# Kernel tuning notes

Hardware: AMD Instinct MI355X
Metric: run time of the kernel (lower is better)

Reference implementation:

```python
import jax, jax.numpy as jnp
import numpy as np
import math

N_HEADS = 16

def _ln(x, g, b, eps=1e-5):
    m = jnp.mean(x, axis=-1, keepdims=True)
    v = jnp.var(x, axis=-1, keepdims=True)
    return (x - m) * jax.lax.rsqrt(v + eps) * g + b

def _block(x, ln1_g, ln1_b, ln2_g, ln2_b, wqkv, wo, w1, w2):
    b, k, d = x.shape
    dh = d // N_HEADS
    h = _ln(x, ln1_g, ln1_b)
    qkv = (h @ wqkv).reshape(b, k, 3, N_HEADS, dh)
    q, kk, v = qkv[:, :, 0], qkv[:, :, 1], qkv[:, :, 2]
    scores = jnp.einsum('bqhd,bkhd->bhqk', q, kk) / math.sqrt(dh)
    attn = jax.nn.softmax(scores, axis=-1)
    o = jnp.einsum('bhqk,bkhd->bqhd', attn, v).reshape(b, k, d) @ wo
    x = x + o
    h2 = _ln(x, ln2_g, ln2_b)
    return x + jax.nn.gelu(h2 @ w1) @ w2

def setup_inputs() -> dict:
    key = jax.random.key(0)
    ks = jax.random.split(key, 6)
    b, s, d, dff = 4, 4096, 1024, 4096
    sc = 0.02
    return {
        'x': jax.random.normal(ks[0], (b, s, d), jnp.float32),
        'router_w': jax.random.normal(ks[1], (d,), jnp.float32) * sc,
        'ln1_g': jnp.ones((d,), jnp.float32),
        'ln1_b': jnp.zeros((d,), jnp.float32),
        'ln2_g': jnp.ones((d,), jnp.float32),
        'ln2_b': jnp.zeros((d,), jnp.float32),
        'wqkv': jax.random.normal(ks[2], (d, 3 * d), jnp.float32) * sc,
        'wo': jax.random.normal(ks[3], (d, d), jnp.float32) * sc,
        'w1': jax.random.normal(ks[4], (d, dff), jnp.float32) * sc,
        'w2': jax.random.normal(ks[5], (dff, d), jnp.float32) * sc,
    }

def reference(x, router_w, ln1_g, ln1_b, ln2_g, ln2_b, wqkv, wo, w1, w2):
    b, s, d = x.shape
    K = s // 2  # top_k = int(s * capacity_factor), capacity_factor = 0.5
    logits = x @ router_w                      # [b, s]
    w, idx = jax.lax.top_k(logits, K)          # [b, K]
    order = jnp.argsort(idx, axis=1)           # sort selected tokens by position
    sel = jnp.take_along_axis(idx, order, axis=1)          # [b, K] sorted indices
    fx = jnp.take_along_axis(x, sel[..., None], axis=1)    # gather routed tokens [b, K, d]
    xo = _block(fx, ln1_g, ln1_b, ln2_g, ln2_b, wqkv, wo, w1, w2)
    rw = jnp.take_along_axis(jax.nn.softmax(w, axis=1), order, axis=1)[..., None]  # [b, K, 1]
    batch_idx = jnp.arange(b)[:, None]
    out = x.at[batch_idx, sel].add(rw * xo)    # softmax-weighted scatter-add
    return out
```

## Files before the change

kernel.cpp:

```cpp
#include <hip/hip_runtime.h>
#include <hip/hip_bf16.h>
#include <stdint.h>

typedef __hip_bfloat16 bf16;
typedef __attribute__((ext_vector_type(8))) short short8;
typedef __attribute__((ext_vector_type(4))) float f32x4;

#define B_   4
#define S_   4096
#define D_   1024
#define KSEL 2048
#define DFF  4096
#define NH   16
#define DH   64

static __device__ __forceinline__ void load_lds16(const void* g, void* l) {
  __builtin_amdgcn_global_load_lds((const __attribute__((address_space(1))) void*)g,
                                   (__attribute__((address_space(3))) void*)l,
                                   16, 0, 0);
}

static __device__ __forceinline__ short8 scale8(short8 v, float s) {
  short8 r;
#pragma unroll
  for (int i = 0; i < 8; ++i) {
    unsigned u = ((unsigned)(unsigned short)v[i]) << 16;
    float f = __uint_as_float(u) * s;
    bf16 o = __float2bfloat16(f);
    short t;
    __builtin_memcpy(&t, &o, 2);
    r[i] = t;
  }
  return r;
}

__global__ __launch_bounds__(256)
void copy_router(const float* __restrict__ x, const float* __restrict__ rwts,
                 float* __restrict__ out, float* __restrict__ logits)
{
  int s = blockIdx.x, b = blockIdx.y;
  int tid = threadIdx.x;
  const float4* row = (const float4*)(x + ((size_t)b * S_ + s) * D_);
  float4 v = row[tid];
  ((float4*)(out + ((size_t)b * S_ + s) * D_))[tid] = v;
  float4 rv = ((const float4*)rwts)[tid];
  float p = v.x * rv.x + v.y * rv.y + v.z * rv.z + v.w * rv.w;
  for (int off = 32; off; off >>= 1) p += __shfl_down(p, off, 64);
  __shared__ float wsum[4];
  if ((tid & 63) == 0) wsum[tid >> 6] = p;
  __syncthreads();
  if (tid == 0) logits[(size_t)b * S_ + s] = wsum[0] + wsum[1] + wsum[2] + wsum[3];
}

__global__ __launch_bounds__(1024)
void topk_kernel(const float* __restrict__ logits,
                 int* __restrict__ sel, float* __restrict__ rw)
{
  __shared__ float lg[4096];
  __shared__ unsigned long long keys[4096];
  __shared__ unsigned char flags[4096];
  __shared__ float wsum[16];
  __shared__ int wtot[16];
  __shared__ int woff[17];

  int b = blockIdx.x, tid = threadIdx.x;
  const float* L = logits + (size_t)b * S_;
  for (int i = tid; i < 4096; i += 1024) {
    float v = L[i];
    lg[i] = v;
    unsigned u = __float_as_uint(v);
    u = (u & 0x80000000u) ? ~u : (u | 0x80000000u);
    u = ~u;
    keys[i] = ((unsigned long long)u << 32) | (unsigned)i;
  }
  __syncthreads();
  for (int k = 2; k <= 4096; k <<= 1) {
    for (int j = k >> 1; j > 0; j >>= 1) {
      for (int t = tid; t < 4096; t += 1024) {
        int ixj = t ^ j;
        if (ixj > t) {
          bool up = ((t & k) == 0);
          unsigned long long a = keys[t], c = keys[ixj];
          if ((a > c) == up) { keys[t] = c; keys[ixj] = a; }
        }
      }
      __syncthreads();
    }
  }
  for (int i = tid; i < 4096; i += 1024) flags[i] = 0;
  __syncthreads();
  for (int i = tid; i < KSEL; i += 1024) flags[(int)(keys[i] & 0xFFFFFFFFu)] = 1;
  __syncthreads();
  float m = lg[(int)(keys[0] & 0xFFFFFFFFu)];
  float part = 0.f;
  for (int i = tid; i < KSEL; i += 1024) part += __expf(lg[(int)(keys[i] & 0xFFFFFFFFu)] - m);
  for (int off = 32; off; off >>= 1) part += __shfl_down(part, off, 64);
  if ((tid & 63) == 0) wsum[tid >> 6] = part;
  __syncthreads();
  if (tid == 0) { float t = 0; for (int w = 0; w < 16; ++w) t += wsum[w]; wsum[0] = t; }
  __syncthreads();
  float inv = 1.0f / wsum[0];
  int base = tid * 4;
  int f0 = flags[base], f1 = flags[base + 1], f2 = flags[base + 2], f3 = flags[base + 3];
  int mysum = f0 + f1 + f2 + f3;
  int incl = mysum;
  int lane = tid & 63;
  for (int off = 1; off < 64; off <<= 1) {
    int t = __shfl_up(incl, off, 64);
    if (lane >= off) incl += t;
  }
  if (lane == 63) wtot[tid >> 6] = incl;
  __syncthreads();
  if (tid == 0) { int sacc = 0; for (int w = 0; w < 16; ++w) { woff[w] = sacc; sacc += wtot[w]; } woff[16] = sacc; }
  __syncthreads();
  int p = woff[tid >> 6] + incl - mysum;
  int fl[4] = { f0, f1, f2, f3 };
  for (int q = 0; q < 4; ++q) {
    if (fl[q]) {
      int idx = base + q;
      sel[b * KSEL + p] = idx;
      rw[b * KSEL + p] = __expf(lg[idx] - m) * inv;
      p++;
    }
  }
}

__global__ __launch_bounds__(256)
void ln_kernel(const float* __restrict__ in, const float* __restrict__ x,
               const int* __restrict__ sel,
               const float* __restrict__ g, const float* __restrict__ beta,
               bf16* __restrict__ out, int gather)
{
  int r = blockIdx.x;
  int tid = threadIdx.x;
  const float* src;
  if (gather) {
    int b = r >> 11, t = r & 2047;
    src = x + ((size_t)b * S_ + sel[b * KSEL + t]) * D_;
  } else {
    src = in + (size_t)r * D_;
  }
  float4 v = ((const float4*)src)[tid];
  float s = v.x + v.y + v.z + v.w;
  float sq = v.x * v.x + v.y * v.y + v.z * v.z + v.w * v.w;
  for (int off = 32; off; off >>= 1) { s += __shfl_down(s, off, 64); sq += __shfl_down(sq, off, 64); }
  __shared__ float wsA[4], wsB[4];
  if ((tid & 63) == 0) { wsA[tid >> 6] = s; wsB[tid >> 6] = sq; }
  __syncthreads();
  float stot = wsA[0] + wsA[1] + wsA[2] + wsA[3];
  float sqt  = wsB[0] + wsB[1] + wsB[2] + wsB[3];
  float mean = stot * (1.f / 1024.f);
  float var  = sqt * (1.f / 1024.f) - mean * mean;
  float rs = rsqrtf(var + 1e-5f);
  float4 gv = ((const float4*)g)[tid];
  float4 bv = ((const float4*)beta)[tid];
  bf16* o = out + (size_t)r * D_ + tid * 4;
  o[0] = __float2bfloat16((v.x - mean) * rs * gv.x + bv.x);
  o[1] = __float2bfloat16((v.y - mean) * rs * gv.y + bv.y);
  o[2] = __float2bfloat16((v.z - mean) * rs * gv.z + bv.z);
  o[3] = __float2bfloat16((v.w - mean) * rs * gv.w + bv.w);
}

__global__ __launch_bounds__(256)
void wtrans(const float* __restrict__ in, bf16* __restrict__ out, int K, int N)
{
  __shared__ float tile[32][33];
  int n0 = blockIdx.x * 32, k0 = blockIdx.y * 32;
  int r = threadIdx.x >> 5, c = threadIdx.x & 31;
#pragma unroll
  for (int i = 0; i < 4; ++i)
    tile[r + 8 * i][c] = in[(size_t)(k0 + r + 8 * i) * N + n0 + c];
  __syncthreads();
#pragma unroll
  for (int i = 0; i < 4; ++i)
    out[(size_t)(n0 + r + 8 * i) * K + k0 + c] = __float2bfloat16(tile[c][r + 8 * i]);
}

__global__ __launch_bounds__(256)
void vt_transpose(const bf16* __restrict__ qkv, bf16* __restrict__ vt)
{
  __shared__ bf16 tile[32][33];
  int bh = blockIdx.z;
  int d0 = blockIdx.y * 32;
  int t0 = blockIdx.x * 32;
  int b = bh >> 4, h = bh & 15;
  int r = threadIdx.x >> 5, c = threadIdx.x & 31;
#pragma unroll
  for (int i = 0; i < 4; ++i) {
    int t = t0 + r + 8 * i;
    tile[r + 8 * i][c] = qkv[(size_t)(b * KSEL + t) * 3072 + 2048 + h * 64 + d0 + c];
  }
  __syncthreads();
#pragma unroll
  for (int i = 0; i < 4; ++i) {
    int d = d0 + r + 8 * i;
    vt[((size_t)bh * 64 + d) * KSEL + t0 + c] = tile[c][r + 8 * i];
  }
}

template<int EPI>
__global__ __launch_bounds__(256)
void gemm_bt(const bf16* __restrict__ A, const bf16* __restrict__ Bt,
             float* __restrict__ Cf, bf16* __restrict__ Cb,
             int M, int N, int K,
             const float* __restrict__ xin, const int* __restrict__ sel,
             const float* __restrict__ rw, const float* __restrict__ x1,
             float* __restrict__ outp)
{
  __shared__ bf16 As[128 * 64];
  __shared__ bf16 Bs[128 * 64];
  const int tid = threadIdx.x;
  const int wid = tid >> 6;
  const int lane = tid & 63;
  const int l15 = lane & 15;
  const int quad = lane >> 4;
  const int wm = wid >> 1, wn = wid & 1;
  const int bm = blockIdx.x * 128;
  const int bn = blockIdx.y * 128;

  const int srow = lane >> 3;
  const int sgrp = (lane & 7) ^ srow;

  f32x4 acc[4][4] = {};

  for (int k0 = 0; k0 < K; k0 += 64) {
#pragma unroll
    for (int c2 = 0; c2 < 4; ++c2) {
      int c = wid * 4 + c2;
      const bf16* ga = A + (size_t)(bm + c * 8 + srow) * K + (k0 + sgrp * 8);
      load_lds16(ga, &As[c * 512]);
      const bf16* gb = Bt + (size_t)(bn + c * 8 + srow) * K + (k0 + sgrp * 8);
      load_lds16(gb, &Bs[c * 512]);
    }
    __syncthreads();
#pragma unroll
    for (int ks = 0; ks < 2; ++ks) {
      short8 af[4], bfv[4];
#pragma unroll
      for (int mt = 0; mt < 4; ++mt) {
        int row = wm * 64 + mt * 16 + l15;
        int cg = (ks * 4 + quad) ^ (row & 7);
        af[mt] = *(const short8*)&As[row * 64 + cg * 8];
      }
#pragma unroll
      for (int nt = 0; nt < 4; ++nt) {
        int row = wn * 64 + nt * 16 + l15;
        int cg = (ks * 4 + quad) ^ (row & 7);
        bfv[nt] = *(const short8*)&Bs[row * 64 + cg * 8];
      }
#pragma unroll
      for (int mt = 0; mt < 4; ++mt)
#pragma unroll
        for (int nt = 0; nt < 4; ++nt)
          acc[mt][nt] = __builtin_amdgcn_mfma_f32_16x16x32_bf16(af[mt], bfv[nt], acc[mt][nt], 0, 0, 0);
    }
    __syncthreads();
  }

#pragma unroll
  for (int mt = 0; mt < 4; ++mt) {
#pragma unroll
    for (int r = 0; r < 4; ++r) {
      int gm = bm + wm * 64 + mt * 16 + quad * 4 + r;
      int bb = gm >> 11, tt = gm & 2047;
      int sr = 0; float rwv = 0.f;
      if (EPI == 1 || EPI == 3) sr = sel[bb * KSEL + tt];
      if (EPI == 3) rwv = rw[bb * KSEL + tt];
#pragma unroll
      for (int nt = 0; nt < 4; ++nt) {
        int gn = bn + wn * 64 + nt * 16 + l15;
        float v = acc[mt][nt][r];
        if (EPI == 0) {
          Cb[(size_t)gm * N + gn] = __float2bfloat16(v);
        } else if (EPI == 1) {
          float xv = xin[((size_t)bb * S_ + sr) * D_ + gn];
          Cf[(size_t)gm * N + gn] = xv + v;
        } else if (EPI == 2) {
          float u = v;
          float cc = 0.7978845608028654f * (u + 0.044715f * u * u * u);
          float e = __expf(2.f * cc);
          float th = 1.f - 2.f / (e + 1.f);
          Cb[(size_t)gm * N + gn] = __float2bfloat16(0.5f * u * (1.f + th));
        } else {
          float v2 = rwv * (x1[(size_t)gm * D_ + gn] + v);
          outp[((size_t)bb * S_ + sr) * D_ + gn] += v2;
        }
      }
    }
  }
}

__global__ __launch_bounds__(256)
void flash_kernel(const bf16* __restrict__ qkv, const bf16* __restrict__ vt,
                  bf16* __restrict__ attn_o)
{
  __shared__ bf16 Ks[128 * 64];
  __shared__ bf16 Vs[64 * 128];
  __shared__ bf16 Pbuf[4][32 * 136];
  int qt = blockIdx.x, h = blockIdx.y, b = blockIdx.z;
  int tid = threadIdx.x, wid = tid >> 6, lane = tid & 63;
  int l15 = lane & 15, quad = lane >> 4;
  int q0 = qt * 128 + wid * 32;

  const int srowK = lane >> 3, sgK = lane & 7;
  const int srowV = lane >> 4, sgV = lane & 15;

  short8 qf[2][2];
#pragma unroll
  for (int mt = 0; mt < 2; ++mt)
#pragma unroll
    for (int ks = 0; ks < 2; ++ks) {
      const bf16* p = qkv + (size_t)(b * KSEL + q0 + mt * 16 + l15) * 3072 + h * 64 + ks * 32 + quad * 8;
      qf[mt][ks] = scale8(*(const short8*)p, 0.125f * 1.44269504f);
    }

  f32x4 acc_o[2][4] = {};
  float lsum[2][4] = {};

  const bf16* Vg = vt + (size_t)(b * NH + h) * 64 * KSEL;
  bf16* pb = Pbuf[wid];

  for (int kt = 0; kt < KSEL / 128; ++kt) {
    int tok0 = b * KSEL + kt * 128;
    __syncthreads();
#pragma unroll
    for (int i = 0; i < 4; ++i) {
      int c = wid * 4 + i;
      const bf16* ga = qkv + (size_t)(tok0 + c * 8 + srowK) * 3072 + 1024 + h * 64 + ((sgK ^ srowK) * 8);
      load_lds16(ga, &Ks[c * 512]);
      int vr = c * 4 + srowV;
      const bf16* gv = Vg + (size_t)vr * KSEL + kt * 128 + ((sgV ^ (vr & 7)) * 8);
      load_lds16(gv, &Vs[c * 512]);
    }
    __syncthreads();

    f32x4 s[2][8] = {};
#pragma unroll
    for (int ks = 0; ks < 2; ++ks) {
#pragma unroll
      for (int nt = 0; nt < 8; ++nt) {
        int row = nt * 16 + l15;
        int g = (ks * 4 + quad) ^ (row & 7);
        short8 kf = *(const short8*)&Ks[row * 64 + g * 8];
#pragma unroll
        for (int mt = 0; mt < 2; ++mt)
          s[mt][nt] = __builtin_amdgcn_mfma_f32_16x16x32_bf16(qf[mt][ks], kf, s[mt][nt], 0, 0, 0);
      }
    }
#pragma unroll
    for (int mt = 0; mt < 2; ++mt)
#pragma unroll
      for (int nt = 0; nt < 8; ++nt)
#pragma unroll
        for (int r = 0; r < 4; ++r) {
          float pv = __builtin_amdgcn_exp2f(s[mt][nt][r]);
          lsum[mt][r] += pv;
          pb[(mt * 16 + quad * 4 + r) * 136 + nt * 16 + l15] = __float2bfloat16(pv);
        }
#pragma unroll
    for (int ks4 = 0; ks4 < 4; ++ks4) {
      short8 bfr[4];
#pragma unroll
      for (int n4 = 0; n4 < 4; ++n4) {
        int row = n4 * 16 + l15;
        int g = (ks4 * 4 + quad) ^ (row & 7);
        bfr[n4] = *(const short8*)&Vs[row * 128 + g * 8];
      }
#pragma unroll
      for (int mt = 0; mt < 2; ++mt) {
        short8 af = *(const short8*)&pb[(mt * 16 + l15) * 136 + ks4 * 32 + quad * 8];
#pragma unroll
        for (int n4 = 0; n4 < 4; ++n4)
          acc_o[mt][n4] = __builtin_amdgcn_mfma_f32_16x16x32_bf16(af, bfr[n4], acc_o[mt][n4], 0, 0, 0);
      }
    }
  }
#pragma unroll
  for (int mt = 0; mt < 2; ++mt)
#pragma unroll
    for (int r = 0; r < 4; ++r) {
#pragma unroll
      for (int off = 1; off < 16; off <<= 1)
        lsum[mt][r] += __shfl_xor(lsum[mt][r], off, 64);
    }
#pragma unroll
  for (int mt = 0; mt < 2; ++mt)
#pragma unroll
    for (int r = 0; r < 4; ++r) {
      float invl = 1.0f / lsum[mt][r];
#pragma unroll
      for (int n4 = 0; n4 < 4; ++n4) {
        attn_o[(size_t)(b * KSEL + q0 + mt * 16 + quad * 4 + r) * D_ + h * 64 + n4 * 16 + l15] =
            __float2bfloat16(acc_o[mt][n4][r] * invl);
      }
    }
}

extern "C" void kernel_launch(void* const* d_in, const int* in_sizes, int n_in,
                              void* d_out, int out_size, void* d_ws, size_t ws_size,
                              hipStream_t stream)
{
  const float* x      = (const float*)d_in[0];
  const float* router = (const float*)d_in[1];
  const float* ln1g   = (const float*)d_in[2];
  const float* ln1b   = (const float*)d_in[3];
  const float* ln2g   = (const float*)d_in[4];
  const float* ln2b   = (const float*)d_in[5];
  const float* wqkv   = (const float*)d_in[6];
  const float* wo     = (const float*)d_in[7];
  const float* w1     = (const float*)d_in[8];
  const float* w2     = (const float*)d_in[9];
  float* out = (float*)d_out;
  char* ws = (char*)d_ws;

  float* logits = (float*)(ws + 0);
  int*   sel    = (int*)  (ws + 65536);
  float* rw     = (float*)(ws + 98304);
  bf16* wqkvT   = (bf16*) (ws + 131072);
  bf16* woT     = (bf16*) (ws + 6422528);
  bf16* w1T     = (bf16*) (ws + 8519680);
  bf16* w2T     = (bf16*) (ws + 16908288);
  bf16* regA    = (bf16*) (ws + 25296896);
  bf16* regB    = (bf16*) (ws + 42074112);
  bf16* vtb     = (bf16*) (ws + 42074112 + 50331648);
  float* x1     = (float*)(ws + 109182976);

  copy_router<<<dim3(S_, B_), 256, 0, stream>>>(x, router, out, logits);
  topk_kernel<<<B_, 1024, 0, stream>>>(logits, sel, rw);

  wtrans<<<dim3(3072 / 32, 1024 / 32), 256, 0, stream>>>(wqkv, wqkvT, 1024, 3072);
  wtrans<<<dim3(1024 / 32, 1024 / 32), 256, 0, stream>>>(wo,   woT,   1024, 1024);
  wtrans<<<dim3(4096 / 32, 1024 / 32), 256, 0, stream>>>(w1,   w1T,   1024, 4096);
  wtrans<<<dim3(1024 / 32, 4096 / 32), 256, 0, stream>>>(w2,   w2T,   4096, 1024);

  ln_kernel<<<B_ * KSEL, 256, 0, stream>>>(nullptr, x, sel, ln1g, ln1b, regA, 1);

  gemm_bt<0><<<dim3(64, 24), 256, 0, stream>>>(regA, wqkvT, nullptr, regB, 8192, 3072, 1024,
                                               nullptr, nullptr, nullptr, nullptr, nullptr);
  vt_transpose<<<dim3(KSEL / 32, 2, B_ * NH), 256, 0, stream>>>(regB, vtb);
  flash_kernel<<<dim3(KSEL / 128, NH, B_), 256, 0, stream>>>(regB, vtb, regA);

  gemm_bt<1><<<dim3(64, 8), 256, 0, stream>>>(regA, woT, x1, nullptr, 8192, 1024, 1024,
                                              x, sel, nullptr, nullptr, nullptr);
  ln_kernel<<<B_ * KSEL, 256, 0, stream>>>(x1, nullptr, nullptr, ln2g, ln2b, regA, 0);
  gemm_bt<2><<<dim3(64, 32), 256, 0, stream>>>(regA, w1T, nullptr, regB, 8192, 4096, 1024,
                                               nullptr, nullptr, nullptr, nullptr, nullptr);
  gemm_bt<3><<<dim3(64, 8), 256, 0, stream>>>(regB, w2T, nullptr, nullptr, 8192, 1024, 4096,
                                              nullptr, sel, rw, x1, out);
}
```

Measured before the change: 671.2 us.

## Keep attention probabilities in registers via transposed MFMA and permlane swaps

```diff
diff --git a/kernel.cpp b/kernel.cpp
--- a/kernel.cpp
+++ b/kernel.cpp
@@ -5,6 +5,9 @@
 typedef __hip_bfloat16 bf16;
 typedef __attribute__((ext_vector_type(8))) short short8;
 typedef __attribute__((ext_vector_type(4))) float f32x4;
+typedef __attribute__((ext_vector_type(2))) unsigned uint2v;
+typedef __attribute__((ext_vector_type(4))) unsigned uint4v;
+typedef __attribute__((ext_vector_type(4))) unsigned short ushort4v;
 
 #define B_   4
 #define S_   4096
@@ -32,6 +35,30 @@
     r[i] = t;
   }
   return r;
+}
+
+static __device__ __forceinline__ unsigned cvt_pk_bf16(float lo, float hi) {
+  unsigned r;
+  asm("v_cvt_pk_bf16_f32 %0, %1, %2" : "=v"(r) : "v"(lo), "v"(hi));
+  return r;
+}
+
+static __device__ __forceinline__ void pl32_swap(unsigned &a, unsigned &b) {
+#if __has_builtin(__builtin_amdgcn_permlane32_swap)
+  uint2v r = __builtin_amdgcn_permlane32_swap(a, b, false, false);
+  a = r[0]; b = r[1];
+#else
+  asm("v_permlane32_swap_b32 %0, %1" : "+v"(a), "+v"(b));
+#endif
+}
+
+static __device__ __forceinline__ void pl16_swap(unsigned &a, unsigned &b) {
+#if __has_builtin(__builtin_amdgcn_permlane16_swap)
+  uint2v r = __builtin_amdgcn_permlane16_swap(a, b, false, false);
+  a = r[0]; b = r[1];
+#else
+  asm("v_permlane16_swap_b32 %0, %1" : "+v"(a), "+v"(b));
+#endif
 }
 
 __global__ __launch_bounds__(256)
@@ -296,7 +323,6 @@
 {
   __shared__ bf16 Ks[128 * 64];
   __shared__ bf16 Vs[64 * 128];
-  __shared__ bf16 Pbuf[4][32 * 136];
   int qt = blockIdx.x, h = blockIdx.y, b = blockIdx.z;
   int tid = threadIdx.x, wid = tid >> 6, lane = tid & 63;
   int l15 = lane & 15, quad = lane >> 4;
@@ -314,11 +340,10 @@
       qf[mt][ks] = scale8(*(const short8*)p, 0.125f * 1.44269504f);
     }
 
-  f32x4 acc_o[2][4] = {};
-  float lsum[2][4] = {};
+  f32x4 acc_ot[2][4] = {};
+  float lsum[2] = {};
 
   const bf16* Vg = vt + (size_t)(b * NH + h) * 64 * KSEL;
-  bf16* pb = Pbuf[wid];
 
   for (int kt = 0; kt < KSEL / 128; ++kt) {
     int tok0 = b * KSEL + kt * 128;
@@ -334,66 +359,70 @@
     }
     __syncthreads();
 
-    f32x4 s[2][8] = {};
-#pragma unroll
-    for (int ks = 0; ks < 2; ++ks) {
-#pragma unroll
-      for (int nt = 0; nt < 8; ++nt) {
-        int row = nt * 16 + l15;
-        int g = (ks * 4 + quad) ^ (row & 7);
-        short8 kf = *(const short8*)&Ks[row * 64 + g * 8];
+#pragma unroll
+    for (int ks4 = 0; ks4 < 4; ++ks4) {
+      f32x4 s[2][2] = {};
+#pragma unroll
+      for (int u = 0; u < 2; ++u) {
+        int row = (ks4 * 2 + u) * 16 + l15;
+#pragma unroll
+        for (int ks = 0; ks < 2; ++ks) {
+          int g = (ks * 4 + quad) ^ (row & 7);
+          short8 kf = *(const short8*)&Ks[row * 64 + g * 8];
+#pragma unroll
+          for (int mt = 0; mt < 2; ++mt)
+            s[mt][u] = __builtin_amdgcn_mfma_f32_16x16x32_bf16(kf, qf[mt][ks], s[mt][u], 0, 0, 0);
+        }
+      }
+      short8 pfrag[2];
+#pragma unroll
+      for (int mt = 0; mt < 2; ++mt) {
+        float pA[4], pB[4];
+#pragma unroll
+        for (int r = 0; r < 4; ++r) {
+          pA[r] = __builtin_amdgcn_exp2f(s[mt][0][r]);
+          pB[r] = __builtin_amdgcn_exp2f(s[mt][1][r]);
+          lsum[mt] += pA[r] + pB[r];
+        }
+        unsigned A0 = cvt_pk_bf16(pA[0], pA[1]);
+        unsigned A1 = cvt_pk_bf16(pA[2], pA[3]);
+        unsigned B0 = cvt_pk_bf16(pB[0], pB[1]);
+        unsigned B1 = cvt_pk_bf16(pB[2], pB[3]);
+        pl32_swap(A0, B0); pl16_swap(A0, B0);
+        pl32_swap(A1, B1); pl16_swap(A1, B1);
+        uint4v w; w[0] = A0; w[1] = A1; w[2] = B0; w[3] = B1;
+        pfrag[mt] = __builtin_bit_cast(short8, w);
+      }
+#pragma unroll
+      for (int dt = 0; dt < 4; ++dt) {
+        int row = dt * 16 + l15;
+        int g = (ks4 * 4 + quad) ^ (row & 7);
+        short8 vf = *(const short8*)&Vs[row * 128 + g * 8];
 #pragma unroll
         for (int mt = 0; mt < 2; ++mt)
-          s[mt][nt] = __builtin_amdgcn_mfma_f32_16x16x32_bf16(qf[mt][ks], kf, s[mt][nt], 0, 0, 0);
-      }
-    }
-#pragma unroll
-    for (int mt = 0; mt < 2; ++mt)
-#pragma unroll
-      for (int nt = 0; nt < 8; ++nt)
-#pragma unroll
-        for (int r = 0; r < 4; ++r) {
-          float pv = __builtin_amdgcn_exp2f(s[mt][nt][r]);
-          lsum[mt][r] += pv;
-          pb[(mt * 16 + quad * 4 + r) * 136 + nt * 16 + l15] = __float2bfloat16(pv);
-        }
-#pragma unroll
-    for (int ks4 = 0; ks4 < 4; ++ks4) {
-      short8 bfr[4];
-#pragma unroll
-      for (int n4 = 0; n4 < 4; ++n4) {
-        int row = n4 * 16 + l15;
-        int g = (ks4 * 4 + quad) ^ (row & 7);
-        bfr[n4] = *(const short8*)&Vs[row * 128 + g * 8];
-      }
-#pragma unroll
-      for (int mt = 0; mt < 2; ++mt) {
-        short8 af = *(const short8*)&pb[(mt * 16 + l15) * 136 + ks4 * 32 + quad * 8];
-#pragma unroll
-        for (int n4 = 0; n4 < 4; ++n4)
-          acc_o[mt][n4] = __builtin_amdgcn_mfma_f32_16x16x32_bf16(af, bfr[n4], acc_o[mt][n4], 0, 0, 0);
-      }
-    }
-  }
-#pragma unroll
-  for (int mt = 0; mt < 2; ++mt)
-#pragma unroll
-    for (int r = 0; r < 4; ++r) {
-#pragma unroll
-      for (int off = 1; off < 16; off <<= 1)
-        lsum[mt][r] += __shfl_xor(lsum[mt][r], off, 64);
-    }
-#pragma unroll
-  for (int mt = 0; mt < 2; ++mt)
-#pragma unroll
-    for (int r = 0; r < 4; ++r) {
-      float invl = 1.0f / lsum[mt][r];
-#pragma unroll
-      for (int n4 = 0; n4 < 4; ++n4) {
-        attn_o[(size_t)(b * KSEL + q0 + mt * 16 + quad * 4 + r) * D_ + h * 64 + n4 * 16 + l15] =
-            __float2bfloat16(acc_o[mt][n4][r] * invl);
-      }
-    }
+          acc_ot[mt][dt] = __builtin_amdgcn_mfma_f32_16x16x32_bf16(vf, pfrag[mt], acc_ot[mt][dt], 0, 0, 0);
+      }
+    }
+  }
+#pragma unroll
+  for (int mt = 0; mt < 2; ++mt) {
+    float l = lsum[mt];
+    l += __shfl_xor(l, 16, 64);
+    l += __shfl_xor(l, 32, 64);
+    float invl = 1.0f / l;
+#pragma unroll
+    for (int dt = 0; dt < 4; ++dt) {
+      ushort4v o;
+#pragma unroll
+      for (int r = 0; r < 4; ++r) {
+        bf16 t = __float2bfloat16(acc_ot[mt][dt][r] * invl);
+        unsigned short us;
+        __builtin_memcpy(&us, &t, 2);
+        o[r] = us;
+      }
+      *(ushort4v*)(attn_o + (size_t)(b * KSEL + q0 + mt * 16 + l15) * D_ + h * 64 + dt * 16 + quad * 4) = o;
+    }
+  }
 }
 
 extern "C" void kernel_launch(void* const* d_in, const int* in_sizes, int n_in,
```

Result: faster. 623.2 us (-7.1%).
